# Kernel tuning notes

Measured on AMD Instinct MI355X. Metric: run time of the kernel, lower is better.

Reference implementation:

```python
import jax, jax.numpy as jnp
import numpy as np

N, E, H, B = 100000, 1600000, 64, 256
EPS = 1e-5


def ln(x, g, b):
    mu = jnp.mean(x, axis=-1, keepdims=True)
    var = jnp.mean((x - mu) ** 2, axis=-1, keepdims=True)
    return (x - mu) * jax.lax.rsqrt(var + EPS) * g + b


def gelu(x):
    # torch nn.GELU default is exact (erf) gelu
    return jax.nn.gelu(x, approximate=False)


def setup_inputs() -> dict:
    key = jax.random.key(0)
    ks = iter(jax.random.split(key, 64))
    nk = lambda: next(ks)
    s = 0.1
    p = {}
    p["x"] = jax.random.normal(nk(), (N, 2), jnp.float32)
    p["edge_attr"] = jax.random.normal(nk(), (E, 2), jnp.float32)
    # node_embed: Linear(2,H) LN GELU Linear(H,H) LN GELU (dropout = eval no-op)
    p["ne_w1"] = jax.random.normal(nk(), (2, H), jnp.float32) * s
    p["ne_b1"] = jnp.zeros((H,), jnp.float32)
    p["ne_g1"] = jnp.ones((H,), jnp.float32)
    p["ne_be1"] = jnp.zeros((H,), jnp.float32)
    p["ne_w2"] = jax.random.normal(nk(), (H, H), jnp.float32) * s
    p["ne_b2"] = jnp.zeros((H,), jnp.float32)
    p["ne_g2"] = jnp.ones((H,), jnp.float32)
    p["ne_be2"] = jnp.zeros((H,), jnp.float32)
    # 3 TrackConv layers: message MLP Linear(H+2,H)+LN, conv output LN, and outer per-layer LN
    p["conv_w"] = jax.random.normal(nk(), (3, H + 2, H), jnp.float32) * s
    p["conv_b"] = jnp.zeros((3, H), jnp.float32)
    p["conv_mg"] = jnp.ones((3, H), jnp.float32)
    p["conv_mb"] = jnp.zeros((3, H), jnp.float32)
    p["conv_ng"] = jnp.ones((3, H), jnp.float32)
    p["conv_nb"] = jnp.zeros((3, H), jnp.float32)
    p["out_ng"] = jnp.ones((3, H), jnp.float32)
    p["out_nb"] = jnp.zeros((3, H), jnp.float32)
    # head MLP: Linear(H,H)+LN+ReLU, Linear(H,H//2)+LN+ReLU, Linear(H//2,1)
    p["m_w1"] = jax.random.normal(nk(), (H, H), jnp.float32) * s
    p["m_b1"] = jnp.zeros((H,), jnp.float32)
    p["m_g1"] = jnp.ones((H,), jnp.float32)
    p["m_be1"] = jnp.zeros((H,), jnp.float32)
    p["m_w2"] = jax.random.normal(nk(), (H, H // 2), jnp.float32) * s
    p["m_b2"] = jnp.zeros((H // 2,), jnp.float32)
    p["m_g2"] = jnp.ones((H // 2,), jnp.float32)
    p["m_be2"] = jnp.zeros((H // 2,), jnp.float32)
    p["m_w3"] = jax.random.normal(nk(), (H // 2, 1), jnp.float32) * s
    p["m_b3"] = jnp.zeros((1,), jnp.float32)
    p["edge_index"] = jax.random.randint(nk(), (2, E), 0, N, dtype=jnp.int32)
    p["batch"] = jnp.sort(jax.random.randint(nk(), (N,), 0, B, dtype=jnp.int32))
    return p


def reference(x, edge_attr,
              ne_w1, ne_b1, ne_g1, ne_be1, ne_w2, ne_b2, ne_g2, ne_be2,
              conv_w, conv_b, conv_mg, conv_mb, conv_ng, conv_nb, out_ng, out_nb,
              m_w1, m_b1, m_g1, m_be1, m_w2, m_b2, m_g2, m_be2, m_w3, m_b3,
              edge_index, batch):
    # node embedding (dropout in eval = identity)
    h = gelu(ln(x @ ne_w1 + ne_b1, ne_g1, ne_be1))
    h = gelu(ln(h @ ne_w2 + ne_b2, ne_g2, ne_be2))
    src, dst = edge_index[0], edge_index[1]  # PyG: message from src (x_j), aggregate at dst
    deg = jax.ops.segment_sum(jnp.ones((E,), h.dtype), dst, num_segments=N)
    deg = jnp.maximum(deg, 1.0)[:, None]
    for l in range(3):
        msg_in = jnp.concatenate([h[src], edge_attr], axis=-1)  # [E, H+2]
        msg = gelu(ln(msg_in @ conv_w[l] + conv_b[l], conv_mg[l], conv_mb[l]))  # [E, H]
        agg = jax.ops.segment_sum(msg, dst, num_segments=N) / deg  # mean aggregate
        conv_out = ln(agg + h, conv_ng[l], conv_nb[l])  # TrackConv: norm(out + residual)
        h = h + ln(conv_out, out_ng[l], out_nb[l])  # outer norm + residual
    # global mean pool over graphs
    cnt = jnp.maximum(jax.ops.segment_sum(jnp.ones((N,), h.dtype), batch, num_segments=B), 1.0)[:, None]
    g = jax.ops.segment_sum(h, batch, num_segments=B) / cnt  # [B, H]
    g = jax.nn.relu(ln(g @ m_w1 + m_b1, m_g1, m_be1))
    g = jax.nn.relu(ln(g @ m_w2 + m_b2, m_g2, m_be2))
    return g @ m_w3 + m_b3  # [B, 1]
```

## Files before the change

### kernel.cpp

```cpp
#include <hip/hip_runtime.h>
#include <math.h>


typedef __attribute__((ext_vector_type(8))) short bfrag;
typedef __attribute__((ext_vector_type(4))) float ffrag;
typedef __attribute__((ext_vector_type(4))) int iv4;

template <int CTRL>
__device__ __forceinline__ float dpp_mov(float v) {
  return __int_as_float(
      __builtin_amdgcn_update_dpp(0, __float_as_int(v), CTRL, 0xF, 0xF, true));
}

__device__ __forceinline__ float rsum16(float v) {
  v += dpp_mov<0x128>(v);
  v += dpp_mov<0x124>(v);
  v += dpp_mov<0x122>(v);
  v += dpp_mov<0x121>(v);
  return v;
}

__device__ __forceinline__ float wave_sum64(float v) {
  v = rsum16(v);
  v += __shfl_xor(v, 16, 64);
  v += __shfl_xor(v, 32, 64);
  return v;
}

__device__ __forceinline__ float ln_apply(float t, float g, float b) {
  float s1 = wave_sum64(t);
  float s2 = wave_sum64(t * t);
  float mu = s1 * 0.015625f;
  float var = fmaf(-mu, mu, s2 * 0.015625f);
  return (t - mu) * rsqrtf(var + 1e-5f) * g + b;
}

__device__ __forceinline__ float erf_fast(float x) {
  float ax = fabsf(x);
  float p = fmaf(fmaf(fmaf(fmaf(0.078108f, ax, 0.000972f), ax, 0.230389f),
                      ax, 0.278393f), ax, 1.0f);
  p = p * p;
  p = p * p;
  float r = __builtin_amdgcn_rcpf(p);
  return copysignf(1.0f - r, x);
}

__device__ __forceinline__ float gelu_exact(float v) {
  float half = 0.5f * v;
  return fmaf(half, erf_fast(v * 0.70710678118654752440f), half);
}

__device__ __forceinline__ float lane_bcast(float v, int k) {
  return __uint_as_float(__builtin_amdgcn_readlane(__float_as_uint(v), k));
}

__device__ __forceinline__ short f2bf(float f) {
  union { float f; unsigned u; } v; v.f = f;
  unsigned r = v.u + 0x7fffu + ((v.u >> 16) & 1u);
  return (short)(r >> 16);
}

__global__ __launch_bounds__(256) void k_init1(
    const float* __restrict__ conv_w, ushort* __restrict__ wt,
    const int* __restrict__ ei, int* __restrict__ csr,
    int ne, int oHist) {
  const int bid = blockIdx.x;
  const int tid = threadIdx.x;
  if (bid < oHist) {
    const int i = bid * 256 + tid;
    const int k = i % 96, f = (i / 96) % 64, l = i / (96 * 64);
    const float v = (k < 66) ? conv_w[(size_t)l * 66 * 64 + k * 64 + f] : 0.0f;
    wt[i] = (ushort)f2bf(v);
    return;
  }
  const int i = (bid - oHist) * 256 + tid;
  if (i < ne) atomicAdd(&csr[ei[ne + i]], 1);
}

__global__ __launch_bounds__(1024) void k_scan_fast(int* __restrict__ buf, int n) {
  __shared__ int wsum[16];
  const int tid = threadIdx.x, lane = tid & 63, w = tid >> 6;
  const int chunk = (((n + 1023) / 1024) + 3) & ~3;
  const int a = min(tid * chunk, n), b = min(a + chunk, n);
  const bool full = (a + chunk <= n);
  int s = 0;
  if (full) {
    const int4* p4 = (const int4*)(buf + a);
#pragma unroll 4
    for (int i = 0; i < chunk / 4; i++) {
      int4 v = p4[i];
      s += v.x + v.y + v.z + v.w;
    }
  } else {
    for (int i = a; i < b; i++) s += buf[i];
  }
  int inc = s;
#pragma unroll
  for (int sh = 1; sh < 64; sh <<= 1) {
    int t = __shfl_up(inc, sh, 64);
    if (lane >= sh) inc += t;
  }
  if (lane == 63) wsum[w] = inc;
  __syncthreads();
  int wb = 0;
  for (int j = 0; j < w; j++) wb += wsum[j];
  int excl = wb + inc - s;
  if (full) {
    int4* p4 = (int4*)(buf + a);
#pragma unroll 4
    for (int i = 0; i < chunk / 4; i++) {
      int4 v = p4[i];
      int4 o;
      o.x = excl; excl += v.x;
      o.y = excl; excl += v.y;
      o.z = excl; excl += v.z;
      o.w = excl; excl += v.w;
      p4[i] = o;
    }
  } else {
    for (int i = a; i < b; i++) { int v = buf[i]; buf[i] = excl; excl += v; }
  }
}

__global__ __launch_bounds__(256) void k_combo(
    const int* __restrict__ ei, const float* __restrict__ ea,
    int* __restrict__ cursor, int4* __restrict__ edata,
    const float* __restrict__ x,
    const float* __restrict__ w1, const float* __restrict__ b1,
    const float* __restrict__ g1, const float* __restrict__ be1,
    const float* __restrict__ w2, const float* __restrict__ b2,
    const float* __restrict__ g2, const float* __restrict__ be2,
    float* __restrict__ h, ushort* __restrict__ hb,
    int n_nodes, int ne, int oEmb, int embWaves) {
  const int bid = blockIdx.x;
  const int tid = threadIdx.x;
  if (bid < oEmb) {
    const int i = bid * 256 + tid;
    if (i < ne) {
      const int d = ei[ne + i];
      const int s = ei[i];
      const float2 eav = *(const float2*)(ea + 2 * (size_t)i);
      const unsigned pk = (unsigned)(ushort)f2bf(eav.x) |
                          ((unsigned)(ushort)f2bf(eav.y) << 16);
      const int pos = atomicAdd(&cursor[d], 1);
      iv4 v = {s, (int)pk, d, 0};
      __builtin_nontemporal_store(v, (iv4*)(edata + pos));
    }
    return;
  }
  const int lane = tid & 63;
  const int wid = ((bid - oEmb) * 256 + tid) >> 6;
  const int nw = embWaves;
  float wc[64];
#pragma unroll
  for (int k = 0; k < 64; k++) wc[k] = w2[k * 64 + lane];
  const float w1a = w1[lane], w1b = w1[64 + lane];
  const float vb1 = b1[lane], vg1 = g1[lane], vbe1 = be1[lane];
  const float vb2 = b2[lane], vg2 = g2[lane], vbe2 = be2[lane];
  for (int n = wid; n < n_nodes; n += nw) {
    const float x0 = x[2 * n], x1 = x[2 * n + 1];
    float t = fmaf(x0, w1a, fmaf(x1, w1b, vb1));
    t = gelu_exact(ln_apply(t, vg1, vbe1));
    float a0 = vb2, a1 = 0.f, a2 = 0.f, a3 = 0.f;
#pragma unroll
    for (int k = 0; k < 64; k += 4) {
      a0 = fmaf(lane_bcast(t, k + 0), wc[k + 0], a0);
      a1 = fmaf(lane_bcast(t, k + 1), wc[k + 1], a1);
      a2 = fmaf(lane_bcast(t, k + 2), wc[k + 2], a2);
      a3 = fmaf(lane_bcast(t, k + 3), wc[k + 3], a3);
    }
    float acc = (a0 + a1) + (a2 + a3);
    acc = gelu_exact(ln_apply(acc, vg2, vbe2));
    h[n * 64 + lane] = acc;
    hb[n * 64 + lane] = (ushort)f2bf(acc);
  }
}

__global__ __launch_bounds__(256, 3) void k_edge_packed(
    const ushort* __restrict__ hb_in, float* __restrict__ agg,
    const int4* __restrict__ edata, const ushort* __restrict__ wt,
    const float* __restrict__ bias, const float* __restrict__ mg,
    const float* __restrict__ mb, int nchunks, int ne) {
  __shared__ __align__(16) ushort lwt[64 * 96];
  {
    const uint4* s = (const uint4*)wt;
    uint4* d = (uint4*)lwt;
    for (int i = threadIdx.x; i < 768; i += 256) d[i] = s[i];
  }
  __syncthreads();

  const int lane = threadIdx.x & 63;
  const int grp = lane >> 4, col = lane & 15;
  const int wid = (blockIdx.x * blockDim.x + threadIdx.x) >> 6;
  const int nw = (gridDim.x * blockDim.x) >> 6;

  float vb[4], vg[4], vbb[4];
#pragma unroll
  for (int t = 0; t < 4; t++) {
    const int f = t * 16 + col;
    vb[t] = bias[f]; vg[t] = mg[f]; vbb[t] = mb[f];
  }

  int c = wid;
  if (c >= nchunks) return;
  int4 e = edata[min(16 * c + col, ne - 1)];
  const ushort* hp0 = hb_in + (size_t)e.x * 64 + grp * 8;
  bfrag A0 = *(const bfrag*)(hp0);
  bfrag A1 = *(const bfrag*)(hp0 + 32);

  for (;;) {
    const int rem = min(16, ne - 16 * c);
    const int cn = c + nw;
    const bool more = cn < nchunks;
    const int nslot = more ? min(16 * cn + col, ne - 1) : min(16 * c + col, ne - 1);
    const int4 en = edata[nslot];

    bfrag A2 = {0, 0, 0, 0, 0, 0, 0, 0};
    if (grp == 0) {
      A2[0] = (short)(e.y & 0xffff);
      A2[1] = (short)((unsigned)e.y >> 16);
    }

    ffrag acc[4];
#pragma unroll
    for (int t = 0; t < 4; t++) { ffrag cc = {vb[t], vb[t], vb[t], vb[t]}; acc[t] = cc; }
#pragma unroll
    for (int t = 0; t < 4; t++) {
      const bfrag B = *(const bfrag*)(lwt + (t * 16 + col) * 96 + grp * 8);
      acc[t] = __builtin_amdgcn_mfma_f32_16x16x32_bf16(A0, B, acc[t], 0, 0, 0);
    }
#pragma unroll
    for (int t = 0; t < 4; t++) {
      const bfrag B = *(const bfrag*)(lwt + (t * 16 + col) * 96 + 32 + grp * 8);
      acc[t] = __builtin_amdgcn_mfma_f32_16x16x32_bf16(A1, B, acc[t], 0, 0, 0);
    }
#pragma unroll
    for (int t = 0; t < 4; t++) {
      const bfrag B = *(const bfrag*)(lwt + (t * 16 + col) * 96 + 64 + grp * 8);
      acc[t] = __builtin_amdgcn_mfma_f32_16x16x32_bf16(A2, B, acc[t], 0, 0, 0);
    }

    const ushort* hq = hb_in + (size_t)en.x * 64 + grp * 8;
    const bfrag N0 = *(const bfrag*)(hq);
    const bfrag N1 = *(const bfrag*)(hq + 32);

    float sx[4], sq[4];
#pragma unroll
    for (int r = 0; r < 4; r++) {
      float s = (acc[0][r] + acc[1][r]) + (acc[2][r] + acc[3][r]);
      float q = fmaf(acc[0][r], acc[0][r], fmaf(acc[1][r], acc[1][r],
                fmaf(acc[2][r], acc[2][r], acc[3][r] * acc[3][r])));
      sx[r] = s; sq[r] = q;
    }
#pragma unroll
    for (int r = 0; r < 4; r++) sx[r] = rsum16(sx[r]);
#pragma unroll
    for (int r = 0; r < 4; r++) sq[r] = rsum16(sq[r]);
    float iv[4], mi[4];
#pragma unroll
    for (int r = 0; r < 4; r++) {
      const float mu = sx[r] * 0.015625f;
      const float var = fmaf(-mu, mu, sq[r] * 0.015625f);
      iv[r] = rsqrtf(var + 1e-5f);
      mi[r] = -mu * iv[r];
    }

#pragma unroll
    for (int t = 0; t < 4; t++) {
#pragma unroll
      for (int r = 0; r < 4; r++) {
        const float z = fmaf(acc[t][r], iv[r], mi[r]);
        acc[t][r] = gelu_exact(fmaf(z, vg[t], vbb[t]));
      }
    }

    const int prev = __shfl_up(e.z, 1, 64);
    const unsigned long long bal = __ballot((col > 0) && (e.z != prev));
    const unsigned bm = (unsigned)bal & 0xFFFEu;

    int s0 = 0;
    while (s0 < rem) {
      const unsigned rest = bm >> (s0 + 1);
      int s1 = rest ? (s0 + 1 + __builtin_ctz(rest)) : 16;
      if (s1 > rem) s1 = rem;
      const int dseg = __builtin_amdgcn_readlane(e.z, s0);
#pragma unroll
      for (int t = 0; t < 4; t++) {
        float rs = 0.f;
#pragma unroll
        for (int r = 0; r < 4; r++) {
          const int row = grp * 4 + r;
          const float w = (row >= s0 && row < s1) ? 1.0f : 0.0f;
          rs = fmaf(acc[t][r], w, rs);
        }
        rs += __shfl_xor(rs, 16, 64);
        rs += __shfl_xor(rs, 32, 64);
        if (lane < 16)
          atomicAdd(&agg[(size_t)dseg * 64 + t * 16 + lane], rs);
      }
      s0 = s1;
    }

    if (!more) break;
    c = cn; e = en; A0 = N0; A1 = N1;
  }
}

__global__ void k_node_update(float* __restrict__ h, ushort* __restrict__ hb,
                              float* __restrict__ agg, const int* __restrict__ ends,
                              const float* __restrict__ ng, const float* __restrict__ nb,
                              const float* __restrict__ og, const float* __restrict__ ob,
                              int n_nodes, int writeHb) {
  const int lane = threadIdx.x & 63;
  const int n = (blockIdx.x * blockDim.x + threadIdx.x) >> 6;
  if (n >= n_nodes) return;
  int start, end;
  if (n == 0) { start = 0; end = ends[0]; }
  else { const int2 se = *(const int2*)(ends + n - 1); start = se.x; end = se.y; }
  const float dg = fmaxf((float)(end - start), 1.0f);
  const float hv = h[(size_t)n * 64 + lane];
  const float a = agg[(size_t)n * 64 + lane] / dg + hv;
  if (writeHb) agg[(size_t)n * 64 + lane] = 0.0f;
  const float c = ln_apply(a, ng[lane], nb[lane]);
  const float o = ln_apply(c, og[lane], ob[lane]);
  const float outv = hv + o;
  h[(size_t)n * 64 + lane] = outv;
  if (writeHb) hb[(size_t)n * 64 + lane] = (ushort)f2bf(outv);
}

__global__ void k_pool_seg(const float* __restrict__ h, const int* __restrict__ batch,
                           float* __restrict__ g, float* __restrict__ cnt,
                           int n_nodes, int chunk) {
  const int lane = threadIdx.x & 63;
  const int wid = (blockIdx.x * blockDim.x + threadIdx.x) >> 6;
  const int n0 = wid * chunk;
  if (n0 >= n_nodes) return;
  const int n1 = min(n0 + chunk, n_nodes);
  int cur = batch[n0], c = 0;
  float acc = 0.f;
  for (int n = n0; n < n1; n++) {
    const int b = batch[n];
    if (b != cur) {
      atomicAdd(&g[(size_t)cur * 64 + lane], acc);
      if (lane == 0) atomicAdd(&cnt[cur], (float)c);
      acc = 0.f; c = 0; cur = b;
    }
    acc += h[(size_t)n * 64 + lane];
    c++;
  }
  atomicAdd(&g[(size_t)cur * 64 + lane], acc);
  if (lane == 0) atomicAdd(&cnt[cur], (float)c);
}

__global__ void k_head(const float* __restrict__ g, const float* __restrict__ cnt,
                       const float* __restrict__ w1, const float* __restrict__ b1,
                       const float* __restrict__ g1, const float* __restrict__ be1,
                       const float* __restrict__ w2, const float* __restrict__ b2,
                       const float* __restrict__ g2, const float* __restrict__ be2,
                       const float* __restrict__ w3, const float* __restrict__ b3,
                       float* __restrict__ out, int nb_) {
  const int lane = threadIdx.x & 63;
  const int row = (blockIdx.x * blockDim.x + threadIdx.x) >> 6;
  if (row >= nb_) return;
  const float c = fmaxf(cnt[row], 1.0f);
  const float gv = g[row * 64 + lane] / c;
  float a0 = b1[lane], a1 = 0.f, a2 = 0.f, a3 = 0.f;
#pragma unroll
  for (int k = 0; k < 64; k += 4) {
    a0 = fmaf(lane_bcast(gv, k + 0), w1[(k + 0) * 64 + lane], a0);
    a1 = fmaf(lane_bcast(gv, k + 1), w1[(k + 1) * 64 + lane], a1);
    a2 = fmaf(lane_bcast(gv, k + 2), w1[(k + 2) * 64 + lane], a2);
    a3 = fmaf(lane_bcast(gv, k + 3), w1[(k + 3) * 64 + lane], a3);
  }
  float t = (a0 + a1) + (a2 + a3);
  t = fmaxf(ln_apply(t, g1[lane], be1[lane]), 0.0f);

  const int j = lane & 31;
  float c0 = b2[j], c1 = 0.f, c2 = 0.f, c3 = 0.f;
#pragma unroll
  for (int k = 0; k < 64; k += 4) {
    c0 = fmaf(lane_bcast(t, k + 0), w2[(k + 0) * 32 + j], c0);
    c1 = fmaf(lane_bcast(t, k + 1), w2[(k + 1) * 32 + j], c1);
    c2 = fmaf(lane_bcast(t, k + 2), w2[(k + 2) * 32 + j], c2);
    c3 = fmaf(lane_bcast(t, k + 3), w2[(k + 3) * 32 + j], c3);
  }
  float t2 = (c0 + c1) + (c2 + c3);
  t2 = fmaxf(ln_apply(t2, g2[j], be2[j]), 0.0f);
  const float p = t2 * w3[j];
  const float s = wave_sum64(p) * 0.5f;
  if (lane == 0) out[row] = s + b3[0];
}

extern "C" void kernel_launch(void* const* d_in, const int* in_sizes, int n_in,
                              void* d_out, int out_size, void* d_ws, size_t ws_size,
                              hipStream_t stream) {
  const float* x      = (const float*)d_in[0];
  const float* ea     = (const float*)d_in[1];
  const float* ne_w1  = (const float*)d_in[2];
  const float* ne_b1  = (const float*)d_in[3];
  const float* ne_g1  = (const float*)d_in[4];
  const float* ne_be1 = (const float*)d_in[5];
  const float* ne_w2  = (const float*)d_in[6];
  const float* ne_b2  = (const float*)d_in[7];
  const float* ne_g2  = (const float*)d_in[8];
  const float* ne_be2 = (const float*)d_in[9];
  const float* conv_w = (const float*)d_in[10];
  const float* conv_b = (const float*)d_in[11];
  const float* conv_mg= (const float*)d_in[12];
  const float* conv_mb= (const float*)d_in[13];
  const float* conv_ng= (const float*)d_in[14];
  const float* conv_nb= (const float*)d_in[15];
  const float* out_ng = (const float*)d_in[16];
  const float* out_nb = (const float*)d_in[17];
  const float* m_w1   = (const float*)d_in[18];
  const float* m_b1   = (const float*)d_in[19];
  const float* m_g1   = (const float*)d_in[20];
  const float* m_be1  = (const float*)d_in[21];
  const float* m_w2   = (const float*)d_in[22];
  const float* m_b2   = (const float*)d_in[23];
  const float* m_g2   = (const float*)d_in[24];
  const float* m_be2  = (const float*)d_in[25];
  const float* m_w3   = (const float*)d_in[26];
  const float* m_b3   = (const float*)d_in[27];
  const int*   eidx   = (const int*)d_in[28];
  const int*   batch  = (const int*)d_in[29];
  float* outp = (float*)d_out;

  const int NN = in_sizes[29];
  const int NE = in_sizes[1] / 2;
  const int NB = out_size;
  const int NCH = (NE + 15) / 16;

  char* wsb = (char*)d_ws;
  float*  h    = (float*)wsb;
  ushort* hb   = (ushort*)(h + (size_t)NN * 64);
  int4*   edata= (int4*)((char*)hb + ((size_t)NN * 128 + 15) / 16 * 16);
  ushort* wt   = (ushort*)(edata + NE);
  float*  gbuf = (float*)(wt + 3 * 64 * 96);
  float*  cnt  = gbuf + (size_t)NB * 64;
  int*    csr  = (int*)(cnt + NB);
  float*  agg  = (float*)((char*)(csr + NN) +
                          (((size_t)(uintptr_t)(csr + NN) & 15) ? 16 - ((size_t)(uintptr_t)(csr + NN) & 15) : 0));

  const dim3 blk(256);

  const size_t zbytes = (char*)(agg + (size_t)NN * 64) - (char*)gbuf;
  hipMemsetAsync(gbuf, 0, zbytes, stream);

  const int nPrep = (3 * 64 * 96) / 256;
  const int nHist = (NE + 255) / 256;
  k_init1<<<nPrep + nHist, blk, 0, stream>>>(conv_w, wt, eidx, csr, NE, nPrep);

  k_scan_fast<<<1, 1024, 0, stream>>>(csr, NN);

  const int nScat = (NE + 255) / 256;
  const int embBlocks = 2048;
  k_combo<<<nScat + embBlocks, blk, 0, stream>>>(
      eidx, ea, csr, edata, x,
      ne_w1, ne_b1, ne_g1, ne_be1, ne_w2, ne_b2, ne_g2, ne_be2,
      h, hb, NN, NE, nScat, embBlocks * 4);

  for (int l = 0; l < 3; l++) {
    k_edge_packed<<<4096, blk, 0, stream>>>(
        hb, agg, edata, wt + (size_t)l * 64 * 96,
        conv_b + l * 64, conv_mg + l * 64, conv_mb + l * 64, NCH, NE);
    k_node_update<<<(NN * 64 + 255) / 256, blk, 0, stream>>>(
        h, hb, agg, csr, conv_ng + l * 64, conv_nb + l * 64,
        out_ng + l * 64, out_nb + l * 64, NN, (l < 2) ? 1 : 0);
  }

  {
    const int chunk = 32;
    const int nwaves = (NN + chunk - 1) / chunk;
    const int nblocks = (nwaves * 64 + 255) / 256;
    k_pool_seg<<<nblocks, blk, 0, stream>>>(h, batch, gbuf, cnt, NN, chunk);
  }
  k_head<<<(NB + 3) / 4, blk, 0, stream>>>(gbuf, cnt, m_w1, m_b1, m_g1, m_be1,
                                           m_w2, m_b2, m_g2, m_be2, m_w3, m_b3,
                                           outp, NB);
}
```

Baseline: 761.4 us.

## Partition edge scatter by destination range across XCD-interleaved blocks

Restructures the CSR scatter in the combo kernel so that each block handles a slice of edges but only writes edges whose destination falls in one of 8 node-range roles picked by block index mod 8. The roles appear intended to line up with the round-robin placement of blocks on the XCDs, keeping the atomic cursor updates and edata writes for a destination range within one XCD's L2. Embedding blocks are interleaved into the same grid (8 of every 32 blocks). In exchange, each edge's destination index is read by 8 different blocks, and the nontemporal store becomes a regular store.

```diff
diff --git a/kernel.cpp b/kernel.cpp
--- a/kernel.cpp
+++ b/kernel.cpp
@@ -4,7 +4,6 @@
 
 typedef __attribute__((ext_vector_type(8))) short bfrag;
 typedef __attribute__((ext_vector_type(4))) float ffrag;
-typedef __attribute__((ext_vector_type(4))) int iv4;
 
 template <int CTRL>
 __device__ __forceinline__ float dpp_mov(float v) {
@@ -131,25 +130,32 @@
     const float* __restrict__ w2, const float* __restrict__ b2,
     const float* __restrict__ g2, const float* __restrict__ be2,
     float* __restrict__ h, ushort* __restrict__ hb,
-    int n_nodes, int ne, int oEmb, int embWaves) {
+    int n_nodes, int ne, int nOrd, int embWaves, float roleScale) {
   const int bid = blockIdx.x;
   const int tid = threadIdx.x;
-  if (bid < oEmb) {
-    const int i = bid * 256 + tid;
-    if (i < ne) {
+  const int sub = bid & 31;
+  if (sub < 24) {
+    const int role = bid & 7;
+    const int ord = (bid >> 5) * 3 + (sub >> 3);
+    const int lo = (int)((long long)ord * ne / nOrd);
+    const int hi = (int)((long long)(ord + 1) * ne / nOrd);
+    for (int i = lo + tid; i < hi; i += 256) {
       const int d = ei[ne + i];
-      const int s = ei[i];
-      const float2 eav = *(const float2*)(ea + 2 * (size_t)i);
-      const unsigned pk = (unsigned)(ushort)f2bf(eav.x) |
-                          ((unsigned)(ushort)f2bf(eav.y) << 16);
-      const int pos = atomicAdd(&cursor[d], 1);
-      iv4 v = {s, (int)pk, d, 0};
-      __builtin_nontemporal_store(v, (iv4*)(edata + pos));
+      const int rd = min(7, (int)((float)d * roleScale));
+      if (rd == role) {
+        const int s = ei[i];
+        const float2 eav = *(const float2*)(ea + 2 * (size_t)i);
+        const unsigned pk = (unsigned)(ushort)f2bf(eav.x) |
+                            ((unsigned)(ushort)f2bf(eav.y) << 16);
+        const int pos = atomicAdd(&cursor[d], 1);
+        edata[pos] = make_int4(s, (int)pk, d, 0);
+      }
     }
     return;
   }
   const int lane = tid & 63;
-  const int wid = ((bid - oEmb) * 256 + tid) >> 6;
+  const int eblk = (bid >> 5) * 8 + (sub - 24);
+  const int wid = (eblk * 256 + tid) >> 6;
   const int nw = embWaves;
   float wc[64];
 #pragma unroll
@@ -453,12 +459,13 @@
 
   k_scan_fast<<<1, 1024, 0, stream>>>(csr, NN);
 
-  const int nScat = (NE + 255) / 256;
-  const int embBlocks = 2048;
-  k_combo<<<nScat + embBlocks, blk, 0, stream>>>(
+  const int ngroups = 261;
+  const int nOrd = ngroups * 3;
+  const int nEmb = ngroups * 8;
+  k_combo<<<ngroups * 32, blk, 0, stream>>>(
       eidx, ea, csr, edata, x,
       ne_w1, ne_b1, ne_g1, ne_be1, ne_w2, ne_b2, ne_g2, ne_be2,
-      h, hb, NN, NE, nScat, embBlocks * 4);
+      h, hb, NN, NE, nOrd, nEmb * 4, 8.0f / (float)NN);
 
   for (int l = 0; l < 3; l++) {
     k_edge_packed<<<4096, blk, 0, stream>>>(
```

Result: faster. 738.6 us, median of 2 (-3.0%).

## Fuse global pooling into last node update and interleave scatter with embedding blocks

Applied to the files above, without the earlier changes.

Drops the separate pooling kernel. The last layer's node update now atomically adds its output straight into the per-graph sums and skips writing h, hb and the agg reset. The per-graph node counts move into the init histogram kernel as extra blocks. The combo kernel interleaves edge-scatter and node-embedding blocks 3:1 instead of running them as consecutive ranges, and the scatter store is now a plain store rather than a nontemporal one. The pooling now issues one atomic per node per channel, which raises atomic contention on 256 graph rows, and the number of embedding waves now depends on the edge count.

```diff
diff --git a/kernel.cpp b/kernel.cpp
--- a/kernel.cpp
+++ b/kernel.cpp
@@ -4,7 +4,6 @@
 
 typedef __attribute__((ext_vector_type(8))) short bfrag;
 typedef __attribute__((ext_vector_type(4))) float ffrag;
-typedef __attribute__((ext_vector_type(4))) int iv4;
 
 template <int CTRL>
 __device__ __forceinline__ float dpp_mov(float v) {
@@ -63,7 +62,8 @@
 __global__ __launch_bounds__(256) void k_init1(
     const float* __restrict__ conv_w, ushort* __restrict__ wt,
     const int* __restrict__ ei, int* __restrict__ csr,
-    int ne, int oHist) {
+    const int* __restrict__ batch, float* __restrict__ cnt,
+    int ne, int n_nodes, int oHist, int oBH) {
   const int bid = blockIdx.x;
   const int tid = threadIdx.x;
   if (bid < oHist) {
@@ -73,8 +73,13 @@
     wt[i] = (ushort)f2bf(v);
     return;
   }
-  const int i = (bid - oHist) * 256 + tid;
-  if (i < ne) atomicAdd(&csr[ei[ne + i]], 1);
+  if (bid < oBH) {
+    const int i = (bid - oHist) * 256 + tid;
+    if (i < ne) atomicAdd(&csr[ei[ne + i]], 1);
+    return;
+  }
+  const int i = (bid - oBH) * 256 + tid;
+  if (i < n_nodes) atomicAdd(&cnt[batch[i]], 1.0f);
 }
 
 __global__ __launch_bounds__(1024) void k_scan_fast(int* __restrict__ buf, int n) {
@@ -131,11 +136,13 @@
     const float* __restrict__ w2, const float* __restrict__ b2,
     const float* __restrict__ g2, const float* __restrict__ be2,
     float* __restrict__ h, ushort* __restrict__ hb,
-    int n_nodes, int ne, int oEmb, int embWaves) {
+    int n_nodes, int ne, int embWaves) {
   const int bid = blockIdx.x;
   const int tid = threadIdx.x;
-  if (bid < oEmb) {
-    const int i = bid * 256 + tid;
+  const int sub = bid & 3;
+  if (sub < 3) {
+    const int ord = (bid >> 2) * 3 + sub;
+    const int i = ord * 256 + tid;
     if (i < ne) {
       const int d = ei[ne + i];
       const int s = ei[i];
@@ -143,13 +150,12 @@
       const unsigned pk = (unsigned)(ushort)f2bf(eav.x) |
                           ((unsigned)(ushort)f2bf(eav.y) << 16);
       const int pos = atomicAdd(&cursor[d], 1);
-      iv4 v = {s, (int)pk, d, 0};
-      __builtin_nontemporal_store(v, (iv4*)(edata + pos));
+      edata[pos] = make_int4(s, (int)pk, d, 0);
     }
     return;
   }
   const int lane = tid & 63;
-  const int wid = ((bid - oEmb) * 256 + tid) >> 6;
+  const int wid = ((bid >> 2) * 256 + tid) >> 6;
   const int nw = embWaves;
   float wc[64];
 #pragma unroll
@@ -310,7 +316,8 @@
                               float* __restrict__ agg, const int* __restrict__ ends,
                               const float* __restrict__ ng, const float* __restrict__ nb,
                               const float* __restrict__ og, const float* __restrict__ ob,
-                              int n_nodes, int writeHb) {
+                              const int* __restrict__ batch, float* __restrict__ gbuf,
+                              int n_nodes, int lastLayer) {
   const int lane = threadIdx.x & 63;
   const int n = (blockIdx.x * blockDim.x + threadIdx.x) >> 6;
   if (n >= n_nodes) return;
@@ -320,36 +327,16 @@
   const float dg = fmaxf((float)(end - start), 1.0f);
   const float hv = h[(size_t)n * 64 + lane];
   const float a = agg[(size_t)n * 64 + lane] / dg + hv;
-  if (writeHb) agg[(size_t)n * 64 + lane] = 0.0f;
   const float c = ln_apply(a, ng[lane], nb[lane]);
   const float o = ln_apply(c, og[lane], ob[lane]);
   const float outv = hv + o;
-  h[(size_t)n * 64 + lane] = outv;
-  if (writeHb) hb[(size_t)n * 64 + lane] = (ushort)f2bf(outv);
-}
-
-__global__ void k_pool_seg(const float* __restrict__ h, const int* __restrict__ batch,
-                           float* __restrict__ g, float* __restrict__ cnt,
-                           int n_nodes, int chunk) {
-  const int lane = threadIdx.x & 63;
-  const int wid = (blockIdx.x * blockDim.x + threadIdx.x) >> 6;
-  const int n0 = wid * chunk;
-  if (n0 >= n_nodes) return;
-  const int n1 = min(n0 + chunk, n_nodes);
-  int cur = batch[n0], c = 0;
-  float acc = 0.f;
-  for (int n = n0; n < n1; n++) {
-    const int b = batch[n];
-    if (b != cur) {
-      atomicAdd(&g[(size_t)cur * 64 + lane], acc);
-      if (lane == 0) atomicAdd(&cnt[cur], (float)c);
-      acc = 0.f; c = 0; cur = b;
-    }
-    acc += h[(size_t)n * 64 + lane];
-    c++;
-  }
-  atomicAdd(&g[(size_t)cur * 64 + lane], acc);
-  if (lane == 0) atomicAdd(&cnt[cur], (float)c);
+  if (lastLayer) {
+    atomicAdd(&gbuf[(size_t)batch[n] * 64 + lane], outv);
+  } else {
+    agg[(size_t)n * 64 + lane] = 0.0f;
+    h[(size_t)n * 64 + lane] = outv;
+    hb[(size_t)n * 64 + lane] = (ushort)f2bf(outv);
+  }
 }
 
 __global__ void k_head(const float* __restrict__ g, const float* __restrict__ cnt,
@@ -449,16 +436,18 @@
 
   const int nPrep = (3 * 64 * 96) / 256;
   const int nHist = (NE + 255) / 256;
-  k_init1<<<nPrep + nHist, blk, 0, stream>>>(conv_w, wt, eidx, csr, NE, nPrep);
+  const int nBH   = (NN + 255) / 256;
+  k_init1<<<nPrep + nHist + nBH, blk, 0, stream>>>(
+      conv_w, wt, eidx, csr, batch, cnt, NE, NN, nPrep, nPrep + nHist);
 
   k_scan_fast<<<1, 1024, 0, stream>>>(csr, NN);
 
-  const int nScat = (NE + 255) / 256;
-  const int embBlocks = 2048;
-  k_combo<<<nScat + embBlocks, blk, 0, stream>>>(
+  const int nScatOrd = (NE + 255) / 256;
+  const int ngroups = (nScatOrd + 2) / 3;
+  k_combo<<<ngroups * 4, blk, 0, stream>>>(
       eidx, ea, csr, edata, x,
       ne_w1, ne_b1, ne_g1, ne_be1, ne_w2, ne_b2, ne_g2, ne_be2,
-      h, hb, NN, NE, nScat, embBlocks * 4);
+      h, hb, NN, NE, ngroups * 4);
 
   for (int l = 0; l < 3; l++) {
     k_edge_packed<<<4096, blk, 0, stream>>>(
@@ -466,15 +455,9 @@
         conv_b + l * 64, conv_mg + l * 64, conv_mb + l * 64, NCH, NE);
     k_node_update<<<(NN * 64 + 255) / 256, blk, 0, stream>>>(
         h, hb, agg, csr, conv_ng + l * 64, conv_nb + l * 64,
-        out_ng + l * 64, out_nb + l * 64, NN, (l < 2) ? 1 : 0);
-  }
-
-  {
-    const int chunk = 32;
-    const int nwaves = (NN + chunk - 1) / chunk;
-    const int nblocks = (nwaves * 64 + 255) / 256;
-    k_pool_seg<<<nblocks, blk, 0, stream>>>(h, batch, gbuf, cnt, NN, chunk);
-  }
+        out_ng + l * 64, out_nb + l * 64, batch, gbuf, NN, (l == 2) ? 1 : 0);
+  }
+
   k_head<<<(NB + 3) / 4, blk, 0, stream>>>(gbuf, cnt, m_w1, m_b1, m_g1, m_be1,
                                            m_w2, m_b2, m_g2, m_be2, m_w3, m_b3,
                                            outp, NB);
```

Measured after the change: 931.5 us. 22.3% more time.
